# Optimization experiments

Measured on AMD Instinct MI355X. Metric: run time of the kernel, lower is better.

## Reference

```python
import jax, jax.numpy as jnp
import numpy as np

N = 500000
TOL = 0.01
ALPHA = 0.1
SLOPE = 0.01
EPS = 1e-10


def smooth_relu(x):
    # 0 for x<0; x^2/2 for 0<=x<1; x-1/2 for x>=1 (C1 smooth ReLU)
    return jnp.where(x < 0, 0.0, jnp.where(x < 1, 0.5 * x * x, x - 0.5))


def leaky_relu(x):
    return jnp.where(x >= 0, x, SLOPE * x)


def _xavier(key, shape):
    fan_out, fan_in = shape
    std = np.sqrt(2.0 / (fan_in + fan_out)).astype(np.float32)
    return jax.random.normal(key, shape, dtype=jnp.float32) * std


def setup_inputs() -> dict:
    key = jax.random.key(0)
    ks = jax.random.split(key, 16)
    inp = {
        'X': jax.random.normal(ks[0], (N, 2), dtype=jnp.float32),
        'Xstable': jnp.zeros((N, 2), dtype=jnp.float32),
        'Vl1_w': _xavier(ks[1], (64, 2)),
        'V2x_w': _xavier(ks[2], (64, 2)),
        'V2z_w': _xavier(ks[3], (64, 64)),
        'V3x_w': _xavier(ks[4], (64, 2)),
        'V3z_w': _xavier(ks[5], (64, 64)),
        'Vfx_w': _xavier(ks[6], (1, 2)),
        'Vfz_w': _xavier(ks[7], (1, 64)),
        'f1_w': _xavier(ks[8], (128, 2)),
        'f1_b': jnp.zeros((128,), dtype=jnp.float32),
        'f2_w': _xavier(ks[9], (128, 128)),
        'f2_b': jnp.zeros((128,), dtype=jnp.float32),
        'f3_w': _xavier(ks[10], (128, 128)),
        'f3_b': jnp.zeros((128,), dtype=jnp.float32),
        'f4_w': _xavier(ks[11], (128, 128)),
        'f4_b': jnp.zeros((128,), dtype=jnp.float32),
        'f5_w': _xavier(ks[12], (128, 128)),
        'f5_b': jnp.zeros((128,), dtype=jnp.float32),
        'ff_w': _xavier(ks[13], (2, 128)),
        'ff_b': jnp.zeros((2,), dtype=jnp.float32),
    }
    return inp


def _V_forward(X, Xstable, Vl1_w, V2x_w, V2z_w, V3x_w, V3z_w, Vfx_w, Vfz_w):
    d = X - Xstable                                  # [N,2]
    z1 = smooth_relu(d @ Vl1_w.T)                    # [N,64]
    z2 = smooth_relu(d @ V2x_w.T + z1 @ V2z_w.T)     # [N,64]
    z3 = smooth_relu(d @ V3x_w.T + z2 @ V3z_w.T)     # [N,64]
    zf = smooth_relu(d @ Vfx_w.T + z3 @ Vfz_w.T)     # [N,1]
    vsum = TOL * jnp.sum(d * d, axis=1, keepdims=True)
    return smooth_relu(zf) + vsum                    # [N,1]


def _fhat_forward(X, f1_w, f1_b, f2_w, f2_b, f3_w, f3_b, f4_w, f4_b, f5_w, f5_b, ff_w, ff_b):
    h = leaky_relu(X @ f1_w.T + f1_b)
    h = leaky_relu(h @ f2_w.T + f2_b)
    h = leaky_relu(h @ f3_w.T + f3_b)
    h = leaky_relu(h @ f4_w.T + f4_b)
    h = leaky_relu(h @ f5_w.T + f5_b)
    return h @ ff_w.T + ff_b                         # [N,2]


def reference(X, Xstable, Vl1_w, V2x_w, V2z_w, V3x_w, V3z_w, Vfx_w, Vfz_w,
              f1_w, f1_b, f2_w, f2_b, f3_w, f3_b, f4_w, f4_b, f5_w, f5_b, ff_w, ff_b):
    def Vfn(Xv):
        return _V_forward(Xv, Xstable, Vl1_w, V2x_w, V2z_w, V3x_w, V3z_w, Vfx_w, Vfz_w)

    V, pullback = jax.vjp(Vfn, X)
    gradV = pullback(jnp.ones_like(V))[0]            # dV/dX, [N,2]

    f_hat = _fhat_forward(X, f1_w, f1_b, f2_w, f2_b, f3_w, f3_b,
                          f4_w, f4_b, f5_w, f5_b, ff_w, ff_b)

    Vnorm = jnp.sum(gradV * gradV, axis=1, keepdims=True)      # [N,1]
    fh_V = jnp.sum(f_hat * gradV, axis=1, keepdims=True)       # [N,1]
    f_mul = jax.nn.relu(fh_V + ALPHA * V) / (Vnorm + EPS)      # [N,1]
    f = f_hat - gradV * f_mul                                  # [N,2]
    return f
```

## Files before the change

kernel.cpp:

```cpp
#include <hip/hip_runtime.h>


typedef _Float16 v2h __attribute__((ext_vector_type(2)));
typedef __fp16   v2hf __attribute__((ext_vector_type(2)));
typedef _Float16 v4h __attribute__((ext_vector_type(4)));
typedef _Float16 v8h __attribute__((ext_vector_type(8)));
typedef float    v4f __attribute__((ext_vector_type(4)));

__device__ __forceinline__ v2h cvt_pk(float a, float b){
  v2hf r = __builtin_amdgcn_cvt_pkrtz(a, b);
  union { v2hf f; v2h h; } u; u.f = r;
  return u.h;
}

#define NPTS 500000
#define FH_BLK  ((NPTS + 127) / 128)
#define VN_BLK  ((NPTS + 127) / 128)
#define FUSED_GRID (FH_BLK + VN_BLK)

#define OFF_FW    0
#define OFF_V2Z   65536
#define OFF_V3Z   69632
#define OFF_V2ZT  73728
#define OFF_V3ZT  77824
#define OFF_VL1T  81920
#define OFF_V2XT  82048
#define OFF_V3XT  82176
#define OFF_VFZ   82304
#define OFF_FFW   82368
#define OFF_F1W   82624
#define W16_DATA  82880
#define W16_TOTAL (W16_DATA + 2048)

__device__ __align__(16) _Float16 g_w16[W16_TOTAL];
__device__ __align__(16) float    g_fh[NPTS * 2];
__device__ __align__(16) float4   g_grad[NPTS];

#if defined(__has_builtin)
#if __has_builtin(__builtin_amdgcn_fdot2)
#define FDOT2(a,b,c) __builtin_amdgcn_fdot2((a),(b),(c),false)
#endif
#endif
#ifndef FDOT2
__device__ __forceinline__ float fdot2_fb(v2h a, v2h b, float c){
  return fmaf((float)a.x, (float)b.x, fmaf((float)a.y, (float)b.y, c));
}
#define FDOT2(a,b,c) fdot2_fb((a),(b),(c))
#endif

__device__ __forceinline__ float srelu(float x){
  float c = fminf(fmaxf(x, 0.f), 1.f);
  return c * fmaf(-0.5f, c, x);
}
__device__ __forceinline__ float sreluD(float x){
  return fminf(fmaxf(x, 0.f), 1.f);
}
__device__ __forceinline__ float sreluD_from_z(float z){
  return fminf(sqrtf(2.f * z), 1.f);
}
__device__ __forceinline__ float dot8(v8h a, v8h b, float s){
  const v2h* ap = (const v2h*)&a;
  const v2h* bp = (const v2h*)&b;
  s = FDOT2(ap[0], bp[0], s);
  s = FDOT2(ap[1], bp[1], s);
  s = FDOT2(ap[2], bp[2], s);
  s = FDOT2(ap[3], bp[3], s);
  return s;
}

__device__ __forceinline__ v2h lrelu_pk(float a, float b){
  v2h x = cvt_pk(a, b);
  v2h m = x * (v2h){(_Float16)0.01f, (_Float16)0.01f};
  return __builtin_elementwise_max(x, m);
}
__device__ __forceinline__ v2h srelu_pk(float a, float b){
  v2h x = cvt_pk(a, b);
  const v2h z0 = (v2h){(_Float16)0.f, (_Float16)0.f};
  const v2h o1 = (v2h){(_Float16)1.f, (_Float16)1.f};
  const v2h hf = (v2h){(_Float16)0.5f, (_Float16)0.5f};
  v2h c = __builtin_elementwise_min(__builtin_elementwise_max(x, z0), o1);
  v2h t = x - c * hf;
  return c * t;
}

__global__ __launch_bounds__(256) void prep_kernel(
  const float* __restrict__ f2w, const float* __restrict__ f3w,
  const float* __restrict__ f4w, const float* __restrict__ f5w,
  const float* __restrict__ V2z, const float* __restrict__ V3z,
  const float* __restrict__ Vl1, const float* __restrict__ V2x,
  const float* __restrict__ V3x, const float* __restrict__ Vfz,
  const float* __restrict__ ffw, const float* __restrict__ f1w)
{
  const int i = blockIdx.x * 256 + threadIdx.x;
  if (i >= W16_TOTAL) return;
  if (i >= W16_DATA){ g_w16[i] = (_Float16)0.f; return; }
  float v;
  if (i < 65536){
    const float* W[4] = {f2w, f3w, f4w, f5w};
    v = W[i >> 14][i & 16383];
  } else if (i < 69632)  v = V2z[i - 65536];
  else if (i < 73728)    v = V3z[i - 69632];
  else if (i < 77824){ int r = i - 73728; v = V2z[(r & 63)*64 + (r >> 6)]; }
  else if (i < 81920){ int r = i - 77824; v = V3z[(r & 63)*64 + (r >> 6)]; }
  else if (i < 82048){ int r = i - 81920; v = Vl1[(r & 63)*2 + (r >> 6)]; }
  else if (i < 82176){ int r = i - 82048; v = V2x[(r & 63)*2 + (r >> 6)]; }
  else if (i < 82304){ int r = i - 82176; v = V3x[(r & 63)*2 + (r >> 6)]; }
  else if (i < 82368)    v = Vfz[i - 82304];
  else if (i < 82624)    v = ffw[i - 82368];
  else                   v = f1w[i - 82624];
  g_w16[i] = (_Float16)v;
}

__device__ __forceinline__ void fh_layer(_Float16* H,
    const _Float16* __restrict__ Wl, const float* __restrict__ Bp,
    int w, int lm, int q)
{
  v4f acc[2][8];
#pragma unroll
  for (int mt = 0; mt < 2; ++mt)
#pragma unroll
    for (int nt = 0; nt < 8; ++nt) acc[mt][nt] = (v4f){0.f,0.f,0.f,0.f};

#pragma unroll
  for (int kt = 0; kt < 4; ++kt){
    const int sw = ((kt*4 + q) ^ lm) << 3;
    v8h A0 = *(const v8h*)(Wl + (w*32      + lm)*128 + kt*32 + q*8);
    v8h A1 = *(const v8h*)(Wl + (w*32 + 16 + lm)*128 + kt*32 + q*8);
#pragma unroll
    for (int nt = 0; nt < 8; ++nt){
      v8h B = *(const v8h*)(H + (nt*16 + lm)*128 + sw);
      acc[0][nt] = __builtin_amdgcn_mfma_f32_16x16x32_f16(A0, B, acc[0][nt], 0,0,0);
      acc[1][nt] = __builtin_amdgcn_mfma_f32_16x16x32_f16(A1, B, acc[1][nt], 0,0,0);
    }
  }
  __syncthreads();
#pragma unroll
  for (int mt = 0; mt < 2; ++mt){
    const int o0 = w*32 + mt*16 + q*4;
    const v4f bv = *(const v4f*)(Bp + o0);
    const int coff = (((o0 >> 3) ^ lm) << 3) + (o0 & 7);
#pragma unroll
    for (int nt = 0; nt < 8; ++nt){
      v4h hv;
      *(v2h*)&hv       = lrelu_pk(acc[mt][nt][0] + bv[0], acc[mt][nt][1] + bv[1]);
      *((v2h*)&hv + 1) = lrelu_pk(acc[mt][nt][2] + bv[2], acc[mt][nt][3] + bv[3]);
      *(v4h*)(H + (nt*16 + lm)*128 + coff) = hv;
    }
  }
  __syncthreads();
}

__device__ __forceinline__ void fhat_body(int b, _Float16* H,
  const float* __restrict__ X,
  const float* __restrict__ f1b, const float* __restrict__ f2b,
  const float* __restrict__ f3b, const float* __restrict__ f4b,
  const float* __restrict__ f5b, const float* __restrict__ ffb)
{
  const int t  = threadIdx.x;
  const int w  = t >> 6;
  const int l  = t & 63;
  const int lm = l & 15;
  const int q  = l >> 4;

  {
    const int r = t >> 1, hf = t & 1, rsw = r & 15;
    int g = b*128 + r; if (g > NPTS-1) g = NPTS-1;
    const float2 xv = *(const float2*)(X + g*2);
    v2h xh; xh.x = (_Float16)xv.x; xh.y = (_Float16)xv.y;
#pragma unroll
    for (int c8 = 0; c8 < 8; ++c8){
      const int c = hf*8 + c8;
      const v4f b0 = *(const v4f*)(f1b + c*8);
      const v4f b1 = *(const v4f*)(f1b + c*8 + 4);
      float vv[8];
#pragma unroll
      for (int j = 0; j < 8; ++j){
        const v2h wv = *(const v2h*)(g_w16 + OFF_F1W + (c*8 + j)*2);
        const float bb = (j < 4) ? b0[j] : b1[j-4];
        vv[j] = FDOT2(xh, wv, bb);
      }
      v8h hv;
#pragma unroll
      for (int j2 = 0; j2 < 4; ++j2)
        ((v2h*)&hv)[j2] = lrelu_pk(vv[2*j2], vv[2*j2+1]);
      *(v8h*)(H + r*128 + ((c ^ rsw) << 3)) = hv;
    }
  }
  __syncthreads();

  fh_layer(H, g_w16 + OFF_FW,         f2b, w, lm, q);
  fh_layer(H, g_w16 + OFF_FW + 16384, f3b, w, lm, q);
  fh_layer(H, g_w16 + OFF_FW + 32768, f4b, w, lm, q);
  fh_layer(H, g_w16 + OFF_FW + 49152, f5b, w, lm, q);

  {
    const int r = t >> 1, c = t & 1, rsw = r & 15;
    float s = ffb[c];
    const v8h* wf = (const v8h*)(g_w16 + OFF_FFW + c*128);
#pragma unroll
    for (int ck = 0; ck < 16; ++ck){
      v8h h = *(const v8h*)(H + r*128 + ((ck ^ rsw) << 3));
      s = dot8(h, wf[ck], s);
    }
    const int row = b*128 + r;
    if (row < NPTS) g_fh[row*2 + c] = s;
  }
}

__device__ __forceinline__ void vfwd2_l2(_Float16* zoutA, _Float16* zoutB,
    const _Float16* __restrict__ Wz,
    const _Float16* __restrict__ WxT,
    const _Float16* __restrict__ Wl1T,
    float dA0, float dA1, float dB0, float dB1, int lm, int q)
{
  v4f accA[4], accB[4];
#pragma unroll
  for (int mt = 0; mt < 4; ++mt){
    accA[mt] = (v4f){0.f,0.f,0.f,0.f};
    accB[mt] = (v4f){0.f,0.f,0.f,0.f};
  }
  const int rs = lm & 7;
#pragma unroll
  for (int kt = 0; kt < 2; ++kt){
    v8h w0 = *(const v8h*)(Wl1T + kt*32 + q*8);
    v8h w1 = *(const v8h*)(Wl1T + 64 + kt*32 + q*8);
    v8h BA, BB;
#pragma unroll
    for (int j2 = 0; j2 < 4; ++j2){
      const float a0 = (float)w0[2*j2  ], a1 = (float)w0[2*j2+1];
      const float c0 = (float)w1[2*j2  ], c1 = (float)w1[2*j2+1];
      ((v2h*)&BA)[j2] = srelu_pk(fmaf(dA0,a0,dA1*c0), fmaf(dA0,a1,dA1*c1));
      ((v2h*)&BB)[j2] = srelu_pk(fmaf(dB0,a0,dB1*c0), fmaf(dB0,a1,dB1*c1));
    }
#pragma unroll
    for (int mt = 0; mt < 4; ++mt){
      v8h A = *(const v8h*)(Wz + (mt*16 + lm)*64 + kt*32 + q*8);
      accA[mt] = __builtin_amdgcn_mfma_f32_16x16x32_f16(A, BA, accA[mt], 0,0,0);
      accB[mt] = __builtin_amdgcn_mfma_f32_16x16x32_f16(A, BB, accB[mt], 0,0,0);
    }
  }
#pragma unroll
  for (int mt = 0; mt < 4; ++mt){
    const int o0 = mt*16 + q*4;
    const int off = (((o0 >> 3) ^ rs) << 3) + (o0 & 7);
    float vA[4], vB[4];
#pragma unroll
    for (int reg = 0; reg < 4; ++reg){
      const float wx0 = (float)WxT[o0 + reg];
      const float wx1 = (float)WxT[64 + o0 + reg];
      vA[reg] = accA[mt][reg] + wx0*dA0 + wx1*dA1;
      vB[reg] = accB[mt][reg] + wx0*dB0 + wx1*dB1;
    }
    v4h hA, hB;
    *(v2h*)&hA       = srelu_pk(vA[0], vA[1]);
    *((v2h*)&hA + 1) = srelu_pk(vA[2], vA[3]);
    *(v2h*)&hB       = srelu_pk(vB[0], vB[1]);
    *((v2h*)&hB + 1) = srelu_pk(vB[2], vB[3]);
    *(v4h*)(zoutA + lm*64 + off) = hA;
    *(v4h*)(zoutB + lm*64 + off) = hB;
  }
}

__device__ __forceinline__ void vfwd2(const _Float16* zinA, _Float16* zoutA,
    const _Float16* zinB, _Float16* zoutB,
    const _Float16* __restrict__ Wz, const _Float16* __restrict__ WxT,
    float dA0, float dA1, float dB0, float dB1, int lm, int q)
{
  v4f accA[4], accB[4];
#pragma unroll
  for (int mt = 0; mt < 4; ++mt){
    accA[mt] = (v4f){0.f,0.f,0.f,0.f};
    accB[mt] = (v4f){0.f,0.f,0.f,0.f};
  }
  const int rs = lm & 7;
#pragma unroll
  for (int kt = 0; kt < 2; ++kt){
    const int sw = (((kt*4 + q) ^ rs) << 3);
    v8h BA = *(const v8h*)(zinA + lm*64 + sw);
    v8h BB = *(const v8h*)(zinB + lm*64 + sw);
#pragma unroll
    for (int mt = 0; mt < 4; ++mt){
      v8h A = *(const v8h*)(Wz + (mt*16 + lm)*64 + kt*32 + q*8);
      accA[mt] = __builtin_amdgcn_mfma_f32_16x16x32_f16(A, BA, accA[mt], 0,0,0);
      accB[mt] = __builtin_amdgcn_mfma_f32_16x16x32_f16(A, BB, accB[mt], 0,0,0);
    }
  }
#pragma unroll
  for (int mt = 0; mt < 4; ++mt){
    const int o0 = mt*16 + q*4;
    const int off = (((o0 >> 3) ^ rs) << 3) + (o0 & 7);
    float vA[4], vB[4];
#pragma unroll
    for (int reg = 0; reg < 4; ++reg){
      const float wx0 = (float)WxT[o0 + reg];
      const float wx1 = (float)WxT[64 + o0 + reg];
      vA[reg] = accA[mt][reg] + wx0*dA0 + wx1*dA1;
      vB[reg] = accB[mt][reg] + wx0*dB0 + wx1*dB1;
    }
    v4h hA, hB;
    *(v2h*)&hA       = srelu_pk(vA[0], vA[1]);
    *((v2h*)&hA + 1) = srelu_pk(vA[2], vA[3]);
    *(v2h*)&hB       = srelu_pk(vB[0], vB[1]);
    *((v2h*)&hB + 1) = srelu_pk(vB[2], vB[3]);
    *(v4h*)(zoutA + lm*64 + off) = hA;
    *(v4h*)(zoutB + lm*64 + off) = hB;
  }
}

__device__ __forceinline__ void vbwd2(const _Float16* ginA, _Float16* zioA,
    const _Float16* ginB, _Float16* zioB,
    const _Float16* __restrict__ WT, int lm, int q)
{
  v4f accA[4], accB[4];
#pragma unroll
  for (int mt = 0; mt < 4; ++mt){
    accA[mt] = (v4f){0.f,0.f,0.f,0.f};
    accB[mt] = (v4f){0.f,0.f,0.f,0.f};
  }
  const int rs = lm & 7;
#pragma unroll
  for (int kt = 0; kt < 2; ++kt){
    const int sw = (((kt*4 + q) ^ rs) << 3);
    v8h BA = *(const v8h*)(ginA + lm*64 + sw);
    v8h BB = *(const v8h*)(ginB + lm*64 + sw);
#pragma unroll
    for (int mt = 0; mt < 4; ++mt){
      v8h A = *(const v8h*)(WT + (mt*16 + lm)*64 + kt*32 + q*8);
      accA[mt] = __builtin_amdgcn_mfma_f32_16x16x32_f16(A, BA, accA[mt], 0,0,0);
      accB[mt] = __builtin_amdgcn_mfma_f32_16x16x32_f16(A, BB, accB[mt], 0,0,0);
    }
  }
#pragma unroll
  for (int mt = 0; mt < 4; ++mt){
    const int k0 = mt*16 + q*4;
    const int off = (((k0 >> 3) ^ rs) << 3) + (k0 & 7);
    _Float16* pA = zioA + lm*64 + off;
    _Float16* pB = zioB + lm*64 + off;
    v4h zA = *(const v4h*)pA;
    v4h zB = *(const v4h*)pB;
    float sA0 = accA[mt][0] * sreluD_from_z((float)zA[0]);
    float sA1 = accA[mt][1] * sreluD_from_z((float)zA[1]);
    float sA2 = accA[mt][2] * sreluD_from_z((float)zA[2]);
    float sA3 = accA[mt][3] * sreluD_from_z((float)zA[3]);
    float sB0 = accB[mt][0] * sreluD_from_z((float)zB[0]);
    float sB1 = accB[mt][1] * sreluD_from_z((float)zB[1]);
    float sB2 = accB[mt][2] * sreluD_from_z((float)zB[2]);
    float sB3 = accB[mt][3] * sreluD_from_z((float)zB[3]);
    v4h gA, gB;
    *(v2h*)&gA       = cvt_pk(sA0, sA1);
    *((v2h*)&gA + 1) = cvt_pk(sA2, sA3);
    *(v2h*)&gB       = cvt_pk(sB0, sB1);
    *((v2h*)&gB + 1) = cvt_pk(sB2, sB3);
    *(v4h*)pA = gA;
    *(v4h*)pB = gB;
  }
}

__device__ __forceinline__ void vbwd2_l1(_Float16* zioA, _Float16* zioB,
    const _Float16* __restrict__ WT,
    const _Float16* __restrict__ Wl1T,
    float dA0, float dA1, float dB0, float dB1, int lm, int q)
{
  v4f accA[4], accB[4];
#pragma unroll
  for (int mt = 0; mt < 4; ++mt){
    accA[mt] = (v4f){0.f,0.f,0.f,0.f};
    accB[mt] = (v4f){0.f,0.f,0.f,0.f};
  }
  const int rs = lm & 7;
#pragma unroll
  for (int kt = 0; kt < 2; ++kt){
    const int sw = (((kt*4 + q) ^ rs) << 3);
    v8h BA = *(const v8h*)(zioA + lm*64 + sw);
    v8h BB = *(const v8h*)(zioB + lm*64 + sw);
#pragma unroll
    for (int mt = 0; mt < 4; ++mt){
      v8h A = *(const v8h*)(WT + (mt*16 + lm)*64 + kt*32 + q*8);
      accA[mt] = __builtin_amdgcn_mfma_f32_16x16x32_f16(A, BA, accA[mt], 0,0,0);
      accB[mt] = __builtin_amdgcn_mfma_f32_16x16x32_f16(A, BB, accB[mt], 0,0,0);
    }
  }
#pragma unroll
  for (int mt = 0; mt < 4; ++mt){
    const int k0 = mt*16 + q*4;
    const int off = (((k0 >> 3) ^ rs) << 3) + (k0 & 7);
    v4h w0 = *(const v4h*)(Wl1T + k0);
    v4h w1 = *(const v4h*)(Wl1T + 64 + k0);
    float sA[4], sB[4];
#pragma unroll
    for (int reg = 0; reg < 4; ++reg){
      const float a1A = fmaf(dA0, (float)w0[reg], dA1 * (float)w1[reg]);
      const float a1B = fmaf(dB0, (float)w0[reg], dB1 * (float)w1[reg]);
      sA[reg] = accA[mt][reg] * sreluD(a1A);
      sB[reg] = accB[mt][reg] * sreluD(a1B);
    }
    v4h gA, gB;
    *(v2h*)&gA       = cvt_pk(sA[0], sA[1]);
    *((v2h*)&gA + 1) = cvt_pk(sA[2], sA[3]);
    *(v2h*)&gB       = cvt_pk(sB[0], sB[1]);
    *((v2h*)&gB + 1) = cvt_pk(sB[2], sB[3]);
    *(v4h*)(zioA + lm*64 + off) = gA;
    *(v4h*)(zioB + lm*64 + off) = gB;
  }
}

__device__ __forceinline__ void gacc2(v4f& aGA, v4f& aGB,
    const _Float16* __restrict__ WxTbase,
    const _Float16* ZA, const _Float16* ZB, int lm, int q)
{
  const int rs = lm & 7;
#pragma unroll
  for (int kt = 0; kt < 2; ++kt){
    const int sw = (((kt*4 + q) ^ rs) << 3);
    v8h A  = *(const v8h*)(WxTbase + lm*64 + kt*32 + q*8);
    v8h BA = *(const v8h*)(ZA + lm*64 + sw);
    v8h BB = *(const v8h*)(ZB + lm*64 + sw);
    aGA = __builtin_amdgcn_mfma_f32_16x16x32_f16(A, BA, aGA, 0,0,0);
    aGB = __builtin_amdgcn_mfma_f32_16x16x32_f16(A, BB, aGB, 0,0,0);
  }
}

__device__ __forceinline__ void vnet_body2(int b, char* smem,
  const float* __restrict__ X, const float* __restrict__ Xst,
  const float* __restrict__ Vfx)
{
  const int t  = threadIdx.x;
  const int w  = t >> 6;
  const int l  = t & 63;
  const int lm = l & 15;
  const int q  = l >> 4;
  const int rs = lm & 7;

  _Float16* const ZA2 = (_Float16*)(smem + w*8192);
  _Float16* const ZA3 = ZA2 + 1024;
  _Float16* const ZB2 = ZA2 + 2048;
  _Float16* const ZB3 = ZA2 + 3072;

  const int rowA = b*128 + w*32 + lm;
  const int rowB = rowA + 16;
  const int rcA = rowA < NPTS ? rowA : NPTS-1;
  const int rcB = rowB < NPTS ? rowB : NPTS-1;
  const float2 xA = *(const float2*)(X   + rcA*2);
  const float2 sA = *(const float2*)(Xst + rcA*2);
  const float2 xB = *(const float2*)(X   + rcB*2);
  const float2 sB = *(const float2*)(Xst + rcB*2);
  const float dA0 = xA.x - sA.x, dA1 = xA.y - sA.y;
  const float dB0 = xB.x - sB.x, dB1 = xB.y - sB.y;
  const float vfx0 = Vfx[0], vfx1 = Vfx[1];

  vfwd2_l2(ZA2, ZB2, g_w16 + OFF_V2Z, g_w16 + OFF_V2XT, g_w16 + OFF_VL1T,
           dA0, dA1, dB0, dB1, lm, q);
  vfwd2(ZA2, ZA3, ZB2, ZB3, g_w16 + OFF_V3Z, g_w16 + OFF_V3XT,
        dA0, dA1, dB0, dB1, lm, q);

  float VVrA, sfA, VVrB, sfB;
  {
    v4f aSA = (v4f){0.f,0.f,0.f,0.f};
    v4f aSB = (v4f){0.f,0.f,0.f,0.f};
#pragma unroll
    for (int kt = 0; kt < 2; ++kt){
      const int sw = (((kt*4 + q) ^ rs) << 3);
      v8h A  = *(const v8h*)(g_w16 + OFF_VFZ + lm*64 + kt*32 + q*8);
      v8h BA = *(const v8h*)(ZA3 + lm*64 + sw);
      v8h BB = *(const v8h*)(ZB3 + lm*64 + sw);
      aSA = __builtin_amdgcn_mfma_f32_16x16x32_f16(A, BA, aSA, 0,0,0);
      aSB = __builtin_amdgcn_mfma_f32_16x16x32_f16(A, BB, aSB, 0,0,0);
    }
    const float afA = fmaf(vfx0, dA0, fmaf(vfx1, dA1, aSA[0]));
    const float zfA = srelu(afA);
    VVrA = srelu(zfA) + 0.01f * fmaf(dA0, dA0, dA1*dA1);
    sfA  = sreluD(zfA) * sreluD(afA);
    const float afB = fmaf(vfx0, dB0, fmaf(vfx1, dB1, aSB[0]));
    const float zfB = srelu(afB);
    VVrB = srelu(zfB) + 0.01f * fmaf(dB0, dB0, dB1*dB1);
    sfB  = sreluD(zfB) * sreluD(afB);
  }

#pragma unroll
  for (int cc = 0; cc < 2; ++cc){
    const int c = q*2 + cc;
    const int sw = ((c ^ rs) << 3);
    v8h vf = *(const v8h*)(g_w16 + OFF_VFZ + c*8);
    _Float16* pA = ZA3 + lm*64 + sw;
    _Float16* pB = ZB3 + lm*64 + sw;
    v8h zA = *(const v8h*)pA;
    v8h zB = *(const v8h*)pB;
    v8h uA, uB;
#pragma unroll
    for (int j2 = 0; j2 < 4; ++j2){
      float a0 = (float)vf[2*j2  ] * sreluD_from_z((float)zA[2*j2  ]);
      float a1 = (float)vf[2*j2+1] * sreluD_from_z((float)zA[2*j2+1]);
      float b0 = (float)vf[2*j2  ] * sreluD_from_z((float)zB[2*j2  ]);
      float b1 = (float)vf[2*j2+1] * sreluD_from_z((float)zB[2*j2+1]);
      ((v2h*)&uA)[j2] = cvt_pk(a0, a1);
      ((v2h*)&uB)[j2] = cvt_pk(b0, b1);
    }
    *(v8h*)pA = uA;
    *(v8h*)pB = uB;
  }

  v4f aGA = (v4f){0.f,0.f,0.f,0.f};
  v4f aGB = (v4f){0.f,0.f,0.f,0.f};

  gacc2(aGA, aGB, g_w16 + OFF_V3XT, ZA3, ZB3, lm, q);
  vbwd2(ZA3, ZA2, ZB3, ZB2, g_w16 + OFF_V3ZT, lm, q);
  gacc2(aGA, aGB, g_w16 + OFF_V2XT, ZA2, ZB2, lm, q);
  vbwd2_l1(ZA2, ZB2, g_w16 + OFF_V2ZT, g_w16 + OFF_VL1T,
           dA0, dA1, dB0, dB1, lm, q);
  gacc2(aGA, aGB, g_w16 + OFF_VL1T, ZA2, ZB2, lm, q);

  const float g0A = fmaf(0.02f, dA0, sfA * (vfx0 + aGA[0]));
  const float g1A = fmaf(0.02f, dA1, sfA * (vfx1 + aGA[1]));
  const float g0B = fmaf(0.02f, dB0, sfB * (vfx0 + aGB[0]));
  const float g1B = fmaf(0.02f, dB1, sfB * (vfx1 + aGB[1]));

  if (q == 0){
    if (rowA < NPTS) g_grad[rowA] = make_float4(g0A, g1A, VVrA, 0.f);
    if (rowB < NPTS) g_grad[rowB] = make_float4(g0B, g1B, VVrB, 0.f);
  }
}

__global__ __launch_bounds__(256, 4) void fused_kernel(
  const float* __restrict__ X, const float* __restrict__ Xst,
  const float* __restrict__ Vfx,
  const float* __restrict__ f1b, const float* __restrict__ f2b,
  const float* __restrict__ f3b, const float* __restrict__ f4b,
  const float* __restrict__ f5b, const float* __restrict__ ffb)
{
  __shared__ __align__(16) char smem[32768];
  const int g = blockIdx.x;
  if ((g & 1) == 0){
    fhat_body(g >> 1, (_Float16*)smem, X, f1b, f2b, f3b, f4b, f5b, ffb);
  } else {
    vnet_body2(g >> 1, smem, X, Xst, Vfx);
  }
}

__global__ __launch_bounds__(256) void combine_kernel(float* __restrict__ out)
{
  const int idx = blockIdx.x * 256 + threadIdx.x;
  const int i0 = idx * 2;
  if (i0 >= NPTS) return;
  const float4 fh2 = *(const float4*)(g_fh + i0*2);
  const float4 ga = g_grad[i0];
  const float4 gb = g_grad[i0 + 1];
  float4 o;
  {
    const float Vn  = fmaf(ga.x, ga.x, ga.y*ga.y);
    const float num = fmaf(0.1f, ga.z, fmaf(fh2.x, ga.x, fh2.y*ga.y));
    const float fm  = fmaxf(num, 0.f) / (Vn + 1e-10f);
    o.x = fmaf(-ga.x, fm, fh2.x);
    o.y = fmaf(-ga.y, fm, fh2.y);
  }
  {
    const float Vn  = fmaf(gb.x, gb.x, gb.y*gb.y);
    const float num = fmaf(0.1f, gb.z, fmaf(fh2.z, gb.x, fh2.w*gb.y));
    const float fm  = fmaxf(num, 0.f) / (Vn + 1e-10f);
    o.z = fmaf(-gb.x, fm, fh2.z);
    o.w = fmaf(-gb.y, fm, fh2.w);
  }
  *(float4*)(out + i0*2) = o;
}

extern "C" void kernel_launch(void* const* d_in, const int* in_sizes, int n_in,
                              void* d_out, int out_size, void* d_ws, size_t ws_size,
                              hipStream_t stream)
{
  (void)d_ws; (void)ws_size; (void)n_in; (void)in_sizes; (void)out_size;
  const float* X   = (const float*)d_in[0];
  const float* Xst = (const float*)d_in[1];
  const float* Vl1 = (const float*)d_in[2];
  const float* V2x = (const float*)d_in[3];
  const float* V2z = (const float*)d_in[4];
  const float* V3x = (const float*)d_in[5];
  const float* V3z = (const float*)d_in[6];
  const float* Vfx = (const float*)d_in[7];
  const float* Vfz = (const float*)d_in[8];
  const float* f1w = (const float*)d_in[9];
  const float* f1b = (const float*)d_in[10];
  const float* f2w = (const float*)d_in[11];
  const float* f2b = (const float*)d_in[12];
  const float* f3w = (const float*)d_in[13];
  const float* f3b = (const float*)d_in[14];
  const float* f4w = (const float*)d_in[15];
  const float* f4b = (const float*)d_in[16];
  const float* f5w = (const float*)d_in[17];
  const float* f5b = (const float*)d_in[18];
  const float* ffw = (const float*)d_in[19];
  const float* ffb = (const float*)d_in[20];

  prep_kernel<<<(W16_TOTAL + 255)/256, 256, 0, stream>>>(
      f2w, f3w, f4w, f5w, V2z, V3z, Vl1, V2x, V3x, Vfz, ffw, f1w);
  fused_kernel<<<FUSED_GRID, 256, 0, stream>>>(
      X, Xst, Vfx, f1b, f2b, f3b, f4b, f5b, ffb);
  combine_kernel<<<(NPTS/2 + 255)/256, 256, 0, stream>>>((float*)d_out);
}
```

Before: 308.6 us.

## Halve per-block tile to 64 rows and raise occupancy to 6 blocks per CU

Each fused block now handles 64 points instead of 128. The f-hat MLP tile shrinks to 4 N-tiles, and the V-net path drops its dual A/B row processing so each wave handles 16 rows. Shared memory per block is halved to 16KB, accumulator registers drop, and launch bounds ask for 6 blocks per CU to hide latency. In exchange, each weight fragment loaded from global/L2 is reused over fewer rows, and block count and sync overhead double.

```diff
diff --git a/kernel.cpp b/kernel.cpp
--- a/kernel.cpp
+++ b/kernel.cpp
@@ -14,9 +14,8 @@
 }
 
 #define NPTS 500000
-#define FH_BLK  ((NPTS + 127) / 128)
-#define VN_BLK  ((NPTS + 127) / 128)
-#define FUSED_GRID (FH_BLK + VN_BLK)
+#define FH_BLK  ((NPTS + 63) / 64)
+#define FUSED_GRID (FH_BLK * 2)
 
 #define OFF_FW    0
 #define OFF_V2Z   65536
@@ -115,11 +114,11 @@
     const _Float16* __restrict__ Wl, const float* __restrict__ Bp,
     int w, int lm, int q)
 {
-  v4f acc[2][8];
+  v4f acc[2][4];
 #pragma unroll
   for (int mt = 0; mt < 2; ++mt)
 #pragma unroll
-    for (int nt = 0; nt < 8; ++nt) acc[mt][nt] = (v4f){0.f,0.f,0.f,0.f};
+    for (int nt = 0; nt < 4; ++nt) acc[mt][nt] = (v4f){0.f,0.f,0.f,0.f};
 
 #pragma unroll
   for (int kt = 0; kt < 4; ++kt){
@@ -127,7 +126,7 @@
     v8h A0 = *(const v8h*)(Wl + (w*32      + lm)*128 + kt*32 + q*8);
     v8h A1 = *(const v8h*)(Wl + (w*32 + 16 + lm)*128 + kt*32 + q*8);
 #pragma unroll
-    for (int nt = 0; nt < 8; ++nt){
+    for (int nt = 0; nt < 4; ++nt){
       v8h B = *(const v8h*)(H + (nt*16 + lm)*128 + sw);
       acc[0][nt] = __builtin_amdgcn_mfma_f32_16x16x32_f16(A0, B, acc[0][nt], 0,0,0);
       acc[1][nt] = __builtin_amdgcn_mfma_f32_16x16x32_f16(A1, B, acc[1][nt], 0,0,0);
@@ -140,7 +139,7 @@
     const v4f bv = *(const v4f*)(Bp + o0);
     const int coff = (((o0 >> 3) ^ lm) << 3) + (o0 & 7);
 #pragma unroll
-    for (int nt = 0; nt < 8; ++nt){
+    for (int nt = 0; nt < 4; ++nt){
       v4h hv;
       *(v2h*)&hv       = lrelu_pk(acc[mt][nt][0] + bv[0], acc[mt][nt][1] + bv[1]);
       *((v2h*)&hv + 1) = lrelu_pk(acc[mt][nt][2] + bv[2], acc[mt][nt][3] + bv[3]);
@@ -163,13 +162,13 @@
   const int q  = l >> 4;
 
   {
-    const int r = t >> 1, hf = t & 1, rsw = r & 15;
-    int g = b*128 + r; if (g > NPTS-1) g = NPTS-1;
+    const int r = t >> 2, sub = t & 3, rsw = r & 15;
+    int g = b*64 + r; if (g > NPTS-1) g = NPTS-1;
     const float2 xv = *(const float2*)(X + g*2);
     v2h xh; xh.x = (_Float16)xv.x; xh.y = (_Float16)xv.y;
 #pragma unroll
-    for (int c8 = 0; c8 < 8; ++c8){
-      const int c = hf*8 + c8;
+    for (int c8 = 0; c8 < 4; ++c8){
+      const int c = sub*4 + c8;
       const v4f b0 = *(const v4f*)(f1b + c*8);
       const v4f b1 = *(const v4f*)(f1b + c*8 + 4);
       float vv[8];
@@ -193,7 +192,7 @@
   fh_layer(H, g_w16 + OFF_FW + 32768, f4b, w, lm, q);
   fh_layer(H, g_w16 + OFF_FW + 49152, f5b, w, lm, q);
 
-  {
+  if (t < 128){
     const int r = t >> 1, c = t & 1, rsw = r & 15;
     float s = ffb[c];
     const v8h* wf = (const v8h*)(g_w16 + OFF_FFW + c*128);
@@ -202,182 +201,143 @@
       v8h h = *(const v8h*)(H + r*128 + ((ck ^ rsw) << 3));
       s = dot8(h, wf[ck], s);
     }
-    const int row = b*128 + r;
+    const int row = b*64 + r;
     if (row < NPTS) g_fh[row*2 + c] = s;
   }
 }
 
-__device__ __forceinline__ void vfwd2_l2(_Float16* zoutA, _Float16* zoutB,
+__device__ __forceinline__ void vfwd_l2(_Float16* zout,
     const _Float16* __restrict__ Wz,
     const _Float16* __restrict__ WxT,
     const _Float16* __restrict__ Wl1T,
-    float dA0, float dA1, float dB0, float dB1, int lm, int q)
-{
-  v4f accA[4], accB[4];
-#pragma unroll
-  for (int mt = 0; mt < 4; ++mt){
-    accA[mt] = (v4f){0.f,0.f,0.f,0.f};
-    accB[mt] = (v4f){0.f,0.f,0.f,0.f};
-  }
+    float d0, float d1, int lm, int q)
+{
+  v4f acc[4];
+#pragma unroll
+  for (int mt = 0; mt < 4; ++mt) acc[mt] = (v4f){0.f,0.f,0.f,0.f};
   const int rs = lm & 7;
 #pragma unroll
   for (int kt = 0; kt < 2; ++kt){
     v8h w0 = *(const v8h*)(Wl1T + kt*32 + q*8);
     v8h w1 = *(const v8h*)(Wl1T + 64 + kt*32 + q*8);
-    v8h BA, BB;
+    v8h B;
 #pragma unroll
     for (int j2 = 0; j2 < 4; ++j2){
       const float a0 = (float)w0[2*j2  ], a1 = (float)w0[2*j2+1];
       const float c0 = (float)w1[2*j2  ], c1 = (float)w1[2*j2+1];
-      ((v2h*)&BA)[j2] = srelu_pk(fmaf(dA0,a0,dA1*c0), fmaf(dA0,a1,dA1*c1));
-      ((v2h*)&BB)[j2] = srelu_pk(fmaf(dB0,a0,dB1*c0), fmaf(dB0,a1,dB1*c1));
+      ((v2h*)&B)[j2] = srelu_pk(fmaf(d0,a0,d1*c0), fmaf(d0,a1,d1*c1));
     }
 #pragma unroll
     for (int mt = 0; mt < 4; ++mt){
       v8h A = *(const v8h*)(Wz + (mt*16 + lm)*64 + kt*32 + q*8);
-      accA[mt] = __builtin_amdgcn_mfma_f32_16x16x32_f16(A, BA, accA[mt], 0,0,0);
-      accB[mt] = __builtin_amdgcn_mfma_f32_16x16x32_f16(A, BB, accB[mt], 0,0,0);
+      acc[mt] = __builtin_amdgcn_mfma_f32_16x16x32_f16(A, B, acc[mt], 0,0,0);
     }
   }
 #pragma unroll
   for (int mt = 0; mt < 4; ++mt){
     const int o0 = mt*16 + q*4;
     const int off = (((o0 >> 3) ^ rs) << 3) + (o0 & 7);
-    float vA[4], vB[4];
+    float v[4];
 #pragma unroll
     for (int reg = 0; reg < 4; ++reg){
       const float wx0 = (float)WxT[o0 + reg];
       const float wx1 = (float)WxT[64 + o0 + reg];
-      vA[reg] = accA[mt][reg] + wx0*dA0 + wx1*dA1;
-      vB[reg] = accB[mt][reg] + wx0*dB0 + wx1*dB1;
-    }
-    v4h hA, hB;
-    *(v2h*)&hA       = srelu_pk(vA[0], vA[1]);
-    *((v2h*)&hA + 1) = srelu_pk(vA[2], vA[3]);
-    *(v2h*)&hB       = srelu_pk(vB[0], vB[1]);
-    *((v2h*)&hB + 1) = srelu_pk(vB[2], vB[3]);
-    *(v4h*)(zoutA + lm*64 + off) = hA;
-    *(v4h*)(zoutB + lm*64 + off) = hB;
-  }
-}
-
-__device__ __forceinline__ void vfwd2(const _Float16* zinA, _Float16* zoutA,
-    const _Float16* zinB, _Float16* zoutB,
+      v[reg] = acc[mt][reg] + wx0*d0 + wx1*d1;
+    }
+    v4h h;
+    *(v2h*)&h       = srelu_pk(v[0], v[1]);
+    *((v2h*)&h + 1) = srelu_pk(v[2], v[3]);
+    *(v4h*)(zout + lm*64 + off) = h;
+  }
+}
+
+__device__ __forceinline__ void vfwd(const _Float16* zin, _Float16* zout,
     const _Float16* __restrict__ Wz, const _Float16* __restrict__ WxT,
-    float dA0, float dA1, float dB0, float dB1, int lm, int q)
-{
-  v4f accA[4], accB[4];
-#pragma unroll
-  for (int mt = 0; mt < 4; ++mt){
-    accA[mt] = (v4f){0.f,0.f,0.f,0.f};
-    accB[mt] = (v4f){0.f,0.f,0.f,0.f};
-  }
+    float d0, float d1, int lm, int q)
+{
+  v4f acc[4];
+#pragma unroll
+  for (int mt = 0; mt < 4; ++mt) acc[mt] = (v4f){0.f,0.f,0.f,0.f};
   const int rs = lm & 7;
 #pragma unroll
   for (int kt = 0; kt < 2; ++kt){
     const int sw = (((kt*4 + q) ^ rs) << 3);
-    v8h BA = *(const v8h*)(zinA + lm*64 + sw);
-    v8h BB = *(const v8h*)(zinB + lm*64 + sw);
+    v8h B = *(const v8h*)(zin + lm*64 + sw);
 #pragma unroll
     for (int mt = 0; mt < 4; ++mt){
       v8h A = *(const v8h*)(Wz + (mt*16 + lm)*64 + kt*32 + q*8);
-      accA[mt] = __builtin_amdgcn_mfma_f32_16x16x32_f16(A, BA, accA[mt], 0,0,0);
-      accB[mt] = __builtin_amdgcn_mfma_f32_16x16x32_f16(A, BB, accB[mt], 0,0,0);
+      acc[mt] = __builtin_amdgcn_mfma_f32_16x16x32_f16(A, B, acc[mt], 0,0,0);
     }
   }
 #pragma unroll
   for (int mt = 0; mt < 4; ++mt){
     const int o0 = mt*16 + q*4;
     const int off = (((o0 >> 3) ^ rs) << 3) + (o0 & 7);
-    float vA[4], vB[4];
+    float v[4];
 #pragma unroll
     for (int reg = 0; reg < 4; ++reg){
       const float wx0 = (float)WxT[o0 + reg];
       const float wx1 = (float)WxT[64 + o0 + reg];
-      vA[reg] = accA[mt][reg] + wx0*dA0 + wx1*dA1;
-      vB[reg] = accB[mt][reg] + wx0*dB0 + wx1*dB1;
-    }
-    v4h hA, hB;
-    *(v2h*)&hA       = srelu_pk(vA[0], vA[1]);
-    *((v2h*)&hA + 1) = srelu_pk(vA[2], vA[3]);
-    *(v2h*)&hB       = srelu_pk(vB[0], vB[1]);
-    *((v2h*)&hB + 1) = srelu_pk(vB[2], vB[3]);
-    *(v4h*)(zoutA + lm*64 + off) = hA;
-    *(v4h*)(zoutB + lm*64 + off) = hB;
-  }
-}
-
-__device__ __forceinline__ void vbwd2(const _Float16* ginA, _Float16* zioA,
-    const _Float16* ginB, _Float16* zioB,
+      v[reg] = acc[mt][reg] + wx0*d0 + wx1*d1;
+    }
+    v4h h;
+    *(v2h*)&h       = srelu_pk(v[0], v[1]);
+    *((v2h*)&h + 1) = srelu_pk(v[2], v[3]);
+    *(v4h*)(zout + lm*64 + off) = h;
+  }
+}
+
+__device__ __forceinline__ void vbwd(const _Float16* gin, _Float16* zio,
     const _Float16* __restrict__ WT, int lm, int q)
 {
-  v4f accA[4], accB[4];
-#pragma unroll
-  for (int mt = 0; mt < 4; ++mt){
-    accA[mt] = (v4f){0.f,0.f,0.f,0.f};
-    accB[mt] = (v4f){0.f,0.f,0.f,0.f};
-  }
+  v4f acc[4];
+#pragma unroll
+  for (int mt = 0; mt < 4; ++mt) acc[mt] = (v4f){0.f,0.f,0.f,0.f};
   const int rs = lm & 7;
 #pragma unroll
   for (int kt = 0; kt < 2; ++kt){
     const int sw = (((kt*4 + q) ^ rs) << 3);
-    v8h BA = *(const v8h*)(ginA + lm*64 + sw);
-    v8h BB = *(const v8h*)(ginB + lm*64 + sw);
+    v8h B = *(const v8h*)(gin + lm*64 + sw);
 #pragma unroll
     for (int mt = 0; mt < 4; ++mt){
       v8h A = *(const v8h*)(WT + (mt*16 + lm)*64 + kt*32 + q*8);
-      accA[mt] = __builtin_amdgcn_mfma_f32_16x16x32_f16(A, BA, accA[mt], 0,0,0);
-      accB[mt] = __builtin_amdgcn_mfma_f32_16x16x32_f16(A, BB, accB[mt], 0,0,0);
+      acc[mt] = __builtin_amdgcn_mfma_f32_16x16x32_f16(A, B, acc[mt], 0,0,0);
     }
   }
 #pragma unroll
   for (int mt = 0; mt < 4; ++mt){
     const int k0 = mt*16 + q*4;
     const int off = (((k0 >> 3) ^ rs) << 3) + (k0 & 7);
-    _Float16* pA = zioA + lm*64 + off;
-    _Float16* pB = zioB + lm*64 + off;
-    v4h zA = *(const v4h*)pA;
-    v4h zB = *(const v4h*)pB;
-    float sA0 = accA[mt][0] * sreluD_from_z((float)zA[0]);
-    float sA1 = accA[mt][1] * sreluD_from_z((float)zA[1]);
-    float sA2 = accA[mt][2] * sreluD_from_z((float)zA[2]);
-    float sA3 = accA[mt][3] * sreluD_from_z((float)zA[3]);
-    float sB0 = accB[mt][0] * sreluD_from_z((float)zB[0]);
-    float sB1 = accB[mt][1] * sreluD_from_z((float)zB[1]);
-    float sB2 = accB[mt][2] * sreluD_from_z((float)zB[2]);
-    float sB3 = accB[mt][3] * sreluD_from_z((float)zB[3]);
-    v4h gA, gB;
-    *(v2h*)&gA       = cvt_pk(sA0, sA1);
-    *((v2h*)&gA + 1) = cvt_pk(sA2, sA3);
-    *(v2h*)&gB       = cvt_pk(sB0, sB1);
-    *((v2h*)&gB + 1) = cvt_pk(sB2, sB3);
-    *(v4h*)pA = gA;
-    *(v4h*)pB = gB;
-  }
-}
-
-__device__ __forceinline__ void vbwd2_l1(_Float16* zioA, _Float16* zioB,
+    _Float16* p = zio + lm*64 + off;
+    v4h z = *(const v4h*)p;
+    float s0 = acc[mt][0] * sreluD_from_z((float)z[0]);
+    float s1 = acc[mt][1] * sreluD_from_z((float)z[1]);
+    float s2 = acc[mt][2] * sreluD_from_z((float)z[2]);
+    float s3 = acc[mt][3] * sreluD_from_z((float)z[3]);
+    v4h gg;
+    *(v2h*)&gg       = cvt_pk(s0, s1);
+    *((v2h*)&gg + 1) = cvt_pk(s2, s3);
+    *(v4h*)p = gg;
+  }
+}
+
+__device__ __forceinline__ void vbwd_l1(_Float16* zio,
     const _Float16* __restrict__ WT,
     const _Float16* __restrict__ Wl1T,
-    float dA0, float dA1, float dB0, float dB1, int lm, int q)
-{
-  v4f accA[4], accB[4];
-#pragma unroll
-  for (int mt = 0; mt < 4; ++mt){
-    accA[mt] = (v4f){0.f,0.f,0.f,0.f};
-    accB[mt] = (v4f){0.f,0.f,0.f,0.f};
-  }
+    float d0, float d1, int lm, int q)
+{
+  v4f acc[4];
+#pragma unroll
+  for (int mt = 0; mt < 4; ++mt) acc[mt] = (v4f){0.f,0.f,0.f,0.f};
   const int rs = lm & 7;
 #pragma unroll
   for (int kt = 0; kt < 2; ++kt){
     const int sw = (((kt*4 + q) ^ rs) << 3);
-    v8h BA = *(const v8h*)(zioA + lm*64 + sw);
-    v8h BB = *(const v8h*)(zioB + lm*64 + sw);
+    v8h B = *(const v8h*)(zio + lm*64 + sw);
 #pragma unroll
     for (int mt = 0; mt < 4; ++mt){
       v8h A = *(const v8h*)(WT + (mt*16 + lm)*64 + kt*32 + q*8);
-      accA[mt] = __builtin_amdgcn_mfma_f32_16x16x32_f16(A, BA, accA[mt], 0,0,0);
-      accB[mt] = __builtin_amdgcn_mfma_f32_16x16x32_f16(A, BB, accB[mt], 0,0,0);
+      acc[mt] = __builtin_amdgcn_mfma_f32_16x16x32_f16(A, B, acc[mt], 0,0,0);
     }
   }
 #pragma unroll
@@ -386,41 +346,34 @@
     const int off = (((k0 >> 3) ^ rs) << 3) + (k0 & 7);
     v4h w0 = *(const v4h*)(Wl1T + k0);
     v4h w1 = *(const v4h*)(Wl1T + 64 + k0);
-    float sA[4], sB[4];
+    float s[4];
 #pragma unroll
     for (int reg = 0; reg < 4; ++reg){
-      const float a1A = fmaf(dA0, (float)w0[reg], dA1 * (float)w1[reg]);
-      const float a1B = fmaf(dB0, (float)w0[reg], dB1 * (float)w1[reg]);
-      sA[reg] = accA[mt][reg] * sreluD(a1A);
-      sB[reg] = accB[mt][reg] * sreluD(a1B);
-    }
-    v4h gA, gB;
-    *(v2h*)&gA       = cvt_pk(sA[0], sA[1]);
-    *((v2h*)&gA + 1) = cvt_pk(sA[2], sA[3]);
-    *(v2h*)&gB       = cvt_pk(sB[0], sB[1]);
-    *((v2h*)&gB + 1) = cvt_pk(sB[2], sB[3]);
-    *(v4h*)(zioA + lm*64 + off) = gA;
-    *(v4h*)(zioB + lm*64 + off) = gB;
-  }
-}
-
-__device__ __forceinline__ void gacc2(v4f& aGA, v4f& aGB,
+      const float a1 = fmaf(d0, (float)w0[reg], d1 * (float)w1[reg]);
+      s[reg] = acc[mt][reg] * sreluD(a1);
+    }
+    v4h gg;
+    *(v2h*)&gg       = cvt_pk(s[0], s[1]);
+    *((v2h*)&gg + 1) = cvt_pk(s[2], s[3]);
+    *(v4h*)(zio + lm*64 + off) = gg;
+  }
+}
+
+__device__ __forceinline__ void gacc(v4f& aG,
     const _Float16* __restrict__ WxTbase,
-    const _Float16* ZA, const _Float16* ZB, int lm, int q)
+    const _Float16* Z, int lm, int q)
 {
   const int rs = lm & 7;
 #pragma unroll
   for (int kt = 0; kt < 2; ++kt){
     const int sw = (((kt*4 + q) ^ rs) << 3);
-    v8h A  = *(const v8h*)(WxTbase + lm*64 + kt*32 + q*8);
-    v8h BA = *(const v8h*)(ZA + lm*64 + sw);
-    v8h BB = *(const v8h*)(ZB + lm*64 + sw);
-    aGA = __builtin_amdgcn_mfma_f32_16x16x32_f16(A, BA, aGA, 0,0,0);
-    aGB = __builtin_amdgcn_mfma_f32_16x16x32_f16(A, BB, aGB, 0,0,0);
-  }
-}
-
-__device__ __forceinline__ void vnet_body2(int b, char* smem,
+    v8h A = *(const v8h*)(WxTbase + lm*64 + kt*32 + q*8);
+    v8h B = *(const v8h*)(Z + lm*64 + sw);
+    aG = __builtin_amdgcn_mfma_f32_16x16x32_f16(A, B, aG, 0,0,0);
+  }
+}
+
+__device__ __forceinline__ void vnet_body(int b, char* smem,
   const float* __restrict__ X, const float* __restrict__ Xst,
   const float* __restrict__ Vfx)
 {
@@ -431,49 +384,34 @@
   const int q  = l >> 4;
   const int rs = lm & 7;
 
-  _Float16* const ZA2 = (_Float16*)(smem + w*8192);
-  _Float16* const ZA3 = ZA2 + 1024;
-  _Float16* const ZB2 = ZA2 + 2048;
-  _Float16* const ZB3 = ZA2 + 3072;
-
-  const int rowA = b*128 + w*32 + lm;
-  const int rowB = rowA + 16;
-  const int rcA = rowA < NPTS ? rowA : NPTS-1;
-  const int rcB = rowB < NPTS ? rowB : NPTS-1;
-  const float2 xA = *(const float2*)(X   + rcA*2);
-  const float2 sA = *(const float2*)(Xst + rcA*2);
-  const float2 xB = *(const float2*)(X   + rcB*2);
-  const float2 sB = *(const float2*)(Xst + rcB*2);
-  const float dA0 = xA.x - sA.x, dA1 = xA.y - sA.y;
-  const float dB0 = xB.x - sB.x, dB1 = xB.y - sB.y;
+  _Float16* const Z2 = (_Float16*)(smem + w*4096);
+  _Float16* const Z3 = Z2 + 1024;
+
+  const int row = b*64 + w*16 + lm;
+  const int rc  = row < NPTS ? row : NPTS-1;
+  const float2 x = *(const float2*)(X   + rc*2);
+  const float2 s = *(const float2*)(Xst + rc*2);
+  const float d0 = x.x - s.x, d1 = x.y - s.y;
   const float vfx0 = Vfx[0], vfx1 = Vfx[1];
 
-  vfwd2_l2(ZA2, ZB2, g_w16 + OFF_V2Z, g_w16 + OFF_V2XT, g_w16 + OFF_VL1T,
-           dA0, dA1, dB0, dB1, lm, q);
-  vfwd2(ZA2, ZA3, ZB2, ZB3, g_w16 + OFF_V3Z, g_w16 + OFF_V3XT,
-        dA0, dA1, dB0, dB1, lm, q);
-
-  float VVrA, sfA, VVrB, sfB;
+  vfwd_l2(Z2, g_w16 + OFF_V2Z, g_w16 + OFF_V2XT, g_w16 + OFF_VL1T,
+          d0, d1, lm, q);
+  vfwd(Z2, Z3, g_w16 + OFF_V3Z, g_w16 + OFF_V3XT, d0, d1, lm, q);
+
+  float VVr, sf;
   {
-    v4f aSA = (v4f){0.f,0.f,0.f,0.f};
-    v4f aSB = (v4f){0.f,0.f,0.f,0.f};
+    v4f aS = (v4f){0.f,0.f,0.f,0.f};
 #pragma unroll
     for (int kt = 0; kt < 2; ++kt){
       const int sw = (((kt*4 + q) ^ rs) << 3);
-      v8h A  = *(const v8h*)(g_w16 + OFF_VFZ + lm*64 + kt*32 + q*8);
-      v8h BA = *(const v8h*)(ZA3 + lm*64 + sw);
-      v8h BB = *(const v8h*)(ZB3 + lm*64 + sw);
-      aSA = __builtin_amdgcn_mfma_f32_16x16x32_f16(A, BA, aSA, 0,0,0);
-      aSB = __builtin_amdgcn_mfma_f32_16x16x32_f16(A, BB, aSB, 0,0,0);
-    }
-    const float afA = fmaf(vfx0, dA0, fmaf(vfx1, dA1, aSA[0]));
-    const float zfA = srelu(afA);
-    VVrA = srelu(zfA) + 0.01f * fmaf(dA0, dA0, dA1*dA1);
-    sfA  = sreluD(zfA) * sreluD(afA);
-    const float afB = fmaf(vfx0, dB0, fmaf(vfx1, dB1, aSB[0]));
-    const float zfB = srelu(afB);
-    VVrB = srelu(zfB) + 0.01f * fmaf(dB0, dB0, dB1*dB1);
-    sfB  = sreluD(zfB) * sreluD(afB);
+      v8h A = *(const v8h*)(g_w16 + OFF_VFZ + lm*64 + kt*32 + q*8);
+      v8h B = *(const v8h*)(Z3 + lm*64 + sw);
+      aS = __builtin_amdgcn_mfma_f32_16x16x32_f16(A, B, aS, 0,0,0);
+    }
+    const float af = fmaf(vfx0, d0, fmaf(vfx1, d1, aS[0]));
+    const float zf = srelu(af);
+    VVr = srelu(zf) + 0.01f * fmaf(d0, d0, d1*d1);
+    sf  = sreluD(zf) * sreluD(af);
   }
 
 #pragma unroll
@@ -481,58 +419,46 @@
     const int c = q*2 + cc;
     const int sw = ((c ^ rs) << 3);
     v8h vf = *(const v8h*)(g_w16 + OFF_VFZ + c*8);
-    _Float16* pA = ZA3 + lm*64 + sw;
-    _Float16* pB = ZB3 + lm*64 + sw;
-    v8h zA = *(const v8h*)pA;
-    v8h zB = *(const v8h*)pB;
-    v8h uA, uB;
+    _Float16* p = Z3 + lm*64 + sw;
+    v8h z = *(const v8h*)p;
+    v8h u;
 #pragma unroll
     for (int j2 = 0; j2 < 4; ++j2){
-      float a0 = (float)vf[2*j2  ] * sreluD_from_z((float)zA[2*j2  ]);
-      float a1 = (float)vf[2*j2+1] * sreluD_from_z((float)zA[2*j2+1]);
-      float b0 = (float)vf[2*j2  ] * sreluD_from_z((float)zB[2*j2  ]);
-      float b1 = (float)vf[2*j2+1] * sreluD_from_z((float)zB[2*j2+1]);
-      ((v2h*)&uA)[j2] = cvt_pk(a0, a1);
-      ((v2h*)&uB)[j2] = cvt_pk(b0, b1);
-    }
-    *(v8h*)pA = uA;
-    *(v8h*)pB = uB;
-  }
-
-  v4f aGA = (v4f){0.f,0.f,0.f,0.f};
-  v4f aGB = (v4f){0.f,0.f,0.f,0.f};
-
-  gacc2(aGA, aGB, g_w16 + OFF_V3XT, ZA3, ZB3, lm, q);
-  vbwd2(ZA3, ZA2, ZB3, ZB2, g_w16 + OFF_V3ZT, lm, q);
-  gacc2(aGA, aGB, g_w16 + OFF_V2XT, ZA2, ZB2, lm, q);
-  vbwd2_l1(ZA2, ZB2, g_w16 + OFF_V2ZT, g_w16 + OFF_VL1T,
-           dA0, dA1, dB0, dB1, lm, q);
-  gacc2(aGA, aGB, g_w16 + OFF_VL1T, ZA2, ZB2, lm, q);
-
-  const float g0A = fmaf(0.02f, dA0, sfA * (vfx0 + aGA[0]));
-  const float g1A = fmaf(0.02f, dA1, sfA * (vfx1 + aGA[1]));
-  const float g0B = fmaf(0.02f, dB0, sfB * (vfx0 + aGB[0]));
-  const float g1B = fmaf(0.02f, dB1, sfB * (vfx1 + aGB[1]));
-
-  if (q == 0){
-    if (rowA < NPTS) g_grad[rowA] = make_float4(g0A, g1A, VVrA, 0.f);
-    if (rowB < NPTS) g_grad[rowB] = make_float4(g0B, g1B, VVrB, 0.f);
-  }
-}
-
-__global__ __launch_bounds__(256, 4) void fused_kernel(
+      float a0 = (float)vf[2*j2  ] * sreluD_from_z((float)z[2*j2  ]);
+      float a1 = (float)vf[2*j2+1] * sreluD_from_z((float)z[2*j2+1]);
+      ((v2h*)&u)[j2] = cvt_pk(a0, a1);
+    }
+    *(v8h*)p = u;
+  }
+
+  v4f aG = (v4f){0.f,0.f,0.f,0.f};
+
+  gacc(aG, g_w16 + OFF_V3XT, Z3, lm, q);
+  vbwd(Z3, Z2, g_w16 + OFF_V3ZT, lm, q);
+  gacc(aG, g_w16 + OFF_V2XT, Z2, lm, q);
+  vbwd_l1(Z2, g_w16 + OFF_V2ZT, g_w16 + OFF_VL1T,
+          d0, d1, lm, q);
+  gacc(aG, g_w16 + OFF_VL1T, Z2, lm, q);
+
+  const float g0 = fmaf(0.02f, d0, sf * (vfx0 + aG[0]));
+  const float g1 = fmaf(0.02f, d1, sf * (vfx1 + aG[1]));
+
+  if (q == 0 && row < NPTS) g_grad[row] = make_float4(g0, g1, VVr, 0.f);
+}
+
+__global__ __launch_bounds__(256, 6) void fused_kernel(
   const float* __restrict__ X, const float* __restrict__ Xst,
   const float* __restrict__ Vfx,
   const float* __restrict__ f1b, const float* __restrict__ f2b,
   const float* __restrict__ f3b, const float* __restrict__ f4b,
   const float* __restrict__ f5b, const float* __restrict__ ffb)
 {
-  __shared__ __align__(16) char smem[32768];
+  __shared__ __align__(16) char smem[16384];
   const int g = blockIdx.x;
   if ((g & 1) == 0){
     fhat_body(g >> 1, (_Float16*)smem, X, f1b, f2b, f3b, f4b, f5b, ffb);
   } else {
-    vnet_body2(g >> 1, smem, X, Xst, Vfx);
+    vnet_body(g >> 1, smem, X, Xst, Vfx);
   }
 }
 
```

After: 474.2 us. 1.54x slower.
